# Kernel optimization log

Measured on AMD Instinct MI355X. Metric: run time of the kernel, lower is better.

The kernel has to match this reference:

```python
import jax, jax.numpy as jnp
import numpy as np

FEAT = 256
HID = 256
HEADS = 4
DH = HID // HEADS
SCALE = DH ** (-0.5)


def _linear(x, W, b):
    # torch nn.Linear convention: W is [out, in]
    return jnp.einsum('...i,oi->...o', x, W) + b


def _layernorm(x, gamma, beta, eps=1e-5):
    mu = jnp.mean(x, axis=-1, keepdims=True)
    var = jnp.mean(jnp.square(x - mu), axis=-1, keepdims=True)
    return (x - mu) * jax.lax.rsqrt(var + eps) * gamma + beta


def setup_inputs() -> dict:
    key = jax.random.key(0)
    ks = jax.random.split(key, 16)
    B, N = 4, 2048
    def w(k, shape, fan_in):
        return jax.random.uniform(k, shape, jnp.float32, -1.0, 1.0) / np.sqrt(fan_in)
    return {
        'x0': jax.random.normal(ks[0], (B, N, FEAT), jnp.float32),
        'x1': jax.random.normal(ks[1], (B, N, FEAT), jnp.float32),
        'Wqk': w(ks[2], (HID, FEAT), FEAT), 'bqk': w(ks[3], (HID,), FEAT),
        'Wv': w(ks[4], (HID, FEAT), FEAT), 'bv': w(ks[5], (HID,), FEAT),
        'Wp': w(ks[6], (HID, HID), HID), 'bp': w(ks[7], (HID,), HID),
        'W1': w(ks[8], (FEAT * 2, FEAT + HID), FEAT + HID), 'b1': w(ks[9], (FEAT * 2,), FEAT + HID),
        'gamma': jnp.ones((FEAT * 2,), jnp.float32), 'beta': jnp.zeros((FEAT * 2,), jnp.float32),
        'W2': w(ks[10], (FEAT, FEAT * 2), FEAT * 2), 'b2': w(ks[11], (FEAT,), FEAT * 2),
    }


def _forward(x0, x1, Wqk, bqk, Wv, bv, Wp, bp, W1, b1, gamma, beta, W2, b2):
    B, N0, _ = x0.shape
    N1 = x1.shape[1]

    def heads(t):  # [B, N, HID] -> [B, H, N, DH]
        return t.reshape(t.shape[0], t.shape[1], HEADS, DH).transpose(0, 2, 1, 3)

    qk0 = heads(_linear(x0, Wqk, bqk)) * (SCALE ** 0.5)
    qk1 = heads(_linear(x1, Wqk, bqk)) * (SCALE ** 0.5)
    v0 = heads(_linear(x0, Wv, bv))
    v1 = heads(_linear(x1, Wv, bv))

    sim = jnp.einsum('bhid,bhjd->bhij', qk0, qk1)  # [B,H,N0,N1]
    attn01 = jax.nn.softmax(sim, axis=-1)                      # rows over N1
    attn10 = jax.nn.softmax(sim.transpose(0, 1, 3, 2), axis=-1)  # [B,H,N1,N0], rows over N0

    m0 = jnp.einsum('bhij,bhjd->bhid', attn01, v1)  # [B,H,N0,DH]
    m1 = jnp.einsum('bhij,bhjd->bhid', attn10, v0)  # [B,H,N1,DH]

    def merge(t):  # [B,H,N,DH] -> [B,N,HID]
        return t.transpose(0, 2, 1, 3).reshape(t.shape[0], t.shape[2], HID)

    m0 = _linear(merge(m0), Wp, bp)
    m1 = _linear(merge(m1), Wp, bp)

    def mlp(x, m):
        h = _linear(jnp.concatenate([x, m], axis=-1), W1, b1)
        h = jax.nn.gelu(_layernorm(h, gamma, beta), approximate=False)
        return x + _linear(h, W2, b2)

    return mlp(x0, m0), mlp(x1, m1)


def reference(x0, x1, Wqk, bqk, Wv, bv, Wp, bp, W1, b1, gamma, beta, W2, b2):
    return _forward(x0, x1, Wqk, bqk, Wv, bv, Wp, bp, W1, b1, gamma, beta, W2, b2)
```

## Files before the change

### kernel.cpp

```cpp
#include <hip/hip_runtime.h>
#include <hip/hip_bf16.h>
#include <math.h>

typedef __hip_bfloat16 hbf;
typedef __attribute__((ext_vector_type(8))) short short8;
typedef __attribute__((ext_vector_type(4))) short short4v;
typedef __attribute__((ext_vector_type(4))) float f32x4;

#define ROWS 8192
#define SQSL 0.4246609001440095f
#define COFF 24.0f

__device__ __forceinline__ short f2b(float f) {
    union { hbf h; short s; } u; u.h = __float2bfloat16(f); return u.s;
}
__device__ __forceinline__ float b2f(short s) {
    union { unsigned u; float f; } x;
    x.u = ((unsigned)(unsigned short)s) << 16; return x.f;
}

__global__ __launch_bounds__(256)
void prep(const float* __restrict__ Wqk, const float* __restrict__ Wv,
          const float* __restrict__ Wp, const float* __restrict__ W1,
          const float* __restrict__ W2,
          const float* __restrict__ bp, const float* __restrict__ b1,
          short* __restrict__ wq, short* __restrict__ wv,
          short* __restrict__ w1c, short* __restrict__ w2,
          float* __restrict__ bc)
{
    const int bid = blockIdx.x, tid = threadIdx.x;
    if (bid < 512) {
        const float* src; short* dst; int base; float sc = 1.f;
        if (bid < 64)       { src = Wqk; dst = wq; base = bid;       sc = SQSL; }
        else if (bid < 128) { src = Wv;  dst = wv; base = bid - 64; }
        else if (bid < 384) {
            int i = (bid - 128) * 256 + tid;
            int n = i >> 7, c = (i & 127) * 4;
            if (c < 256) {
                float4 f = ((const float4*)W1)[i];
                short4v s;
                s[0] = f2b(f.x); s[1] = f2b(f.y); s[2] = f2b(f.z); s[3] = f2b(f.w);
                *(short4v*)(w1c + (size_t)n * 512 + c) = s;
            }
            return;
        }
        else                { src = W2;  dst = w2; base = bid - 384; }
        int i = base * 256 + tid;
        float4 f = ((const float4*)src)[i];
        short4v s;
        s[0] = f2b(f.x * sc); s[1] = f2b(f.y * sc);
        s[2] = f2b(f.z * sc); s[3] = f2b(f.w * sc);
        *(short4v*)(dst + (size_t)i * 4) = s;
    } else if (bid < 1024) {
        int n = bid - 512;
        const float* wrow = W1 + (size_t)n * 512 + 256;
        float acc = 0.f;
        for (int k = 0; k < 256; ++k)
            acc += wrow[k] * Wp[(size_t)k * 256 + tid];
        w1c[(size_t)n * 512 + 256 + tid] = f2b(acc);
    } else {
        int n = (bid - 1024) * 256 + tid;
        const float* wrow = W1 + (size_t)n * 512 + 256;
        float acc = b1[n];
        for (int k = 0; k < 256; ++k) acc += wrow[k] * bp[k];
        bc[n] = acc;
    }
}

__global__ __launch_bounds__(256)
void gemm_qkv(const float* __restrict__ x0, const float* __restrict__ x1,
              const short* __restrict__ Wa, const short* __restrict__ Wb,
              const float* __restrict__ bias0, const float* __restrict__ bias1,
              short* __restrict__ Cb, short* __restrict__ Cb2)
{
    const int col0 = blockIdx.x * 128;
    const int row0 = blockIdx.y * 64;
    const int tid = threadIdx.x;
    const int lane = tid & 63, wave = tid >> 6;
    const int ln = lane & 15, quad = lane >> 4;
    const int wm = wave & 1, wn = wave >> 1;

    __shared__ short As[64 * 40];
    __shared__ short Bs[128 * 40];

    const int ar = tid >> 2, ac = tid & 3;

    f32x4 acc[2][4];
    #pragma unroll
    for (int i = 0; i < 2; ++i)
        #pragma unroll
        for (int j = 0; j < 4; ++j) acc[i][j] = {0.f, 0.f, 0.f, 0.f};

    auto wptr = [&](int rr, int kk) -> const short* {
        int n = col0 + rr;
        if (col0 < 256) return Wa + (size_t)n * 256 + kk;
        return Wb + (size_t)(n - 256) * 256 + kk;
    };
    const float* xrow = (row0 + ar < ROWS)
        ? x0 + (size_t)(row0 + ar) * 256
        : x1 + (size_t)(row0 + ar - ROWS) * 256;

    float4 aF0 = ((const float4*)(xrow + ac * 8))[0];
    float4 aF1 = ((const float4*)(xrow + ac * 8))[1];
    short8 bR0 = *(const short8*)wptr(ar, ac * 8);
    short8 bR1 = *(const short8*)wptr(ar + 64, ac * 8);

    for (int k0 = 0; k0 < 256; k0 += 32) {
        {
            short8 s;
            s[0] = f2b(aF0.x); s[1] = f2b(aF0.y); s[2] = f2b(aF0.z); s[3] = f2b(aF0.w);
            s[4] = f2b(aF1.x); s[5] = f2b(aF1.y); s[6] = f2b(aF1.z); s[7] = f2b(aF1.w);
            *(short8*)&As[ar * 40 + ac * 8] = s;
        }
        *(short8*)&Bs[ar * 40 + ac * 8] = bR0;
        *(short8*)&Bs[(ar + 64) * 40 + ac * 8] = bR1;
        __syncthreads();

        if (k0 + 32 < 256) {
            aF0 = ((const float4*)(xrow + k0 + 32 + ac * 8))[0];
            aF1 = ((const float4*)(xrow + k0 + 32 + ac * 8))[1];
            bR0 = *(const short8*)wptr(ar, k0 + 32 + ac * 8);
            bR1 = *(const short8*)wptr(ar + 64, k0 + 32 + ac * 8);
        }

        short8 a[2], b[4];
        #pragma unroll
        for (int mi = 0; mi < 2; ++mi)
            a[mi] = *(const short8*)&As[(wm * 32 + mi * 16 + ln) * 40 + quad * 8];
        #pragma unroll
        for (int nj = 0; nj < 4; ++nj)
            b[nj] = *(const short8*)&Bs[(wn * 64 + nj * 16 + ln) * 40 + quad * 8];
        #pragma unroll
        for (int mi = 0; mi < 2; ++mi)
            #pragma unroll
            for (int nj = 0; nj < 4; ++nj)
                acc[mi][nj] = __builtin_amdgcn_mfma_f32_16x16x32_bf16(
                                  b[nj], a[mi], acc[mi][nj], 0, 0, 0);
        __syncthreads();
    }

    #pragma unroll
    for (int nj = 0; nj < 4; ++nj) {
        int wrel = wn * 64 + nj * 16 + quad * 4;
        int wcol = col0 + wrel;
        const float* bias = (wcol >= 256) ? bias1 : bias0;
        int boff = (wcol >= 256) ? (wcol - 256) : wcol;
        float4 bb = *(const float4*)(bias + boff);
        #pragma unroll
        for (int mi = 0; mi < 2; ++mi) {
            int tok = row0 + wm * 32 + mi * 16 + ln;
            f32x4 v = acc[mi][nj];
            short4v o;
            if (wcol < 256) {
                o[0] = f2b(fmaf(bb.x, SQSL, v[0])); o[1] = f2b(fmaf(bb.y, SQSL, v[1]));
                o[2] = f2b(fmaf(bb.z, SQSL, v[2])); o[3] = f2b(fmaf(bb.w, SQSL, v[3]));
                *(short4v*)(Cb + (size_t)tok * 256 + wcol) = o;
            } else {
                o[0] = f2b(v[0] + bb.x); o[1] = f2b(v[1] + bb.y);
                o[2] = f2b(v[2] + bb.z); o[3] = f2b(v[3] + bb.w);
                *(short4v*)(Cb2 + (size_t)tok * 256 + (wcol - 256)) = o;
            }
        }
    }
}

__global__ __launch_bounds__(256)
void vtrans(const short* __restrict__ vbuf, short* __restrict__ vtbuf)
{
    const int tt = blockIdx.x;
    const int gh = blockIdx.y;
    const int g = gh >> 2, h = gh & 3;
    const int tid = threadIdx.x;
    const int tok0 = g * 2048 + tt * 64;

    __shared__ short Ls[64 * 76];

    {
        int c4 = tid & 15, r0 = tid >> 4;
        #pragma unroll
        for (int gg = 0; gg < 4; ++gg) {
            int r = r0 + gg * 16;
            *(short4v*)&Ls[r * 76 + c4 * 4] =
                *(const short4v*)(vbuf + (size_t)(tok0 + r) * 256 + h * 64 + c4 * 4);
        }
    }
    __syncthreads();

    #pragma unroll
    for (int p = 0; p < 2; ++p) {
        int ch = tid + p * 256;
        int d = ch >> 3, cc = ch & 7;
        short8 s;
        #pragma unroll
        for (int j = 0; j < 8; ++j) s[j] = Ls[(cc * 8 + j) * 76 + d];
        *(short8*)(vtbuf + (size_t)((g * 4 + h) * 64 + d) * 2048 + tt * 64 + cc * 8) = s;
    }
}

__global__ __launch_bounds__(128, 2)
void attn8(const short* __restrict__ qkb, const short* __restrict__ vtbuf,
           short* __restrict__ pO0, short* __restrict__ pO1,
           float* __restrict__ l0, float* __restrict__ l1)
{
    const int qt   = blockIdx.x;
    const int b    = blockIdx.y >> 2, h = blockIdx.y & 3;
    const int dir  = blockIdx.z >> 1;
    const int half = blockIdx.z & 1;
    const int tid = threadIdx.x;
    const int lane = tid & 63, wave = tid >> 6;
    const int ln   = lane & 15, quad = lane >> 4;

    const int qbase = dir * ROWS + b * 2048;
    const int kbase = (1 - dir) * ROWS + b * 2048;
    const int vg    = ((1 - dir) * 4 + b) * 4 + h;
    const int jlo   = half * 1024, jhi = jlo + 1024;

    short* __restrict__ pO = half ? pO1 : pO0;
    float* __restrict__ lb = half ? l1  : l0;

    __shared__ short QP[128 * 72];
    __shared__ short KS[64 * 72];
    __shared__ short VT[64 * 72];

    const int c = tid & 7, r0 = tid >> 3;
    #pragma unroll
    for (int g = 0; g < 8; ++g) {
        int r = r0 + g * 16;
        *(short8*)&QP[r * 72 + c * 8] =
            *(const short8*)(qkb + (size_t)(qbase + qt * 128 + r) * 256 + h * 64 + c * 8);
    }
    #pragma unroll
    for (int g = 0; g < 4; ++g) {
        int r = r0 + g * 16;
        *(short8*)&KS[r * 72 + c * 8] =
            *(const short8*)(qkb + (size_t)(kbase + jlo + r) * 256 + h * 64 + c * 8);
        *(short8*)&VT[r * 72 + c * 8] =
            *(const short8*)(vtbuf + (size_t)(vg * 64 + r) * 2048 + jlo + c * 8);
    }
    __syncthreads();

    short8 qf[4][2];
    #pragma unroll
    for (int mi = 0; mi < 4; ++mi)
        #pragma unroll
        for (int ks = 0; ks < 2; ++ks)
            qf[mi][ks] = *(const short8*)&QP[(wave * 64 + mi * 16 + ln) * 72
                                             + ks * 32 + quad * 8];

    f32x4 Ot[4][4];
    #pragma unroll
    for (int mi = 0; mi < 4; ++mi)
        #pragma unroll
        for (int dt = 0; dt < 4; ++dt) Ot[mi][dt] = {0.f, 0.f, 0.f, 0.f};
    float lrun[4] = {0.f, 0.f, 0.f, 0.f};

    for (int j0 = jlo; j0 < jhi; j0 += 64) {
        short8 kreg[4], vreg[4];
        const bool more = (j0 + 64) < jhi;
        if (more) {
            #pragma unroll
            for (int g = 0; g < 4; ++g) {
                int r = r0 + g * 16;
                kreg[g] = *(const short8*)(qkb + (size_t)(kbase + j0 + 64 + r) * 256
                                           + h * 64 + c * 8);
                vreg[g] = *(const short8*)(vtbuf + (size_t)(vg * 64 + r) * 2048
                                           + j0 + 64 + c * 8);
            }
        }

        f32x4 St[4][4];
        #pragma unroll
        for (int t = 0; t < 4; ++t) {
            short8 k0 = *(const short8*)&KS[(t * 16 + ln) * 72 + quad * 8];
            short8 k1 = *(const short8*)&KS[(t * 16 + ln) * 72 + 32 + quad * 8];
            #pragma unroll
            for (int mi = 0; mi < 4; ++mi) {
                f32x4 z = {0.f, 0.f, 0.f, 0.f};
                z = __builtin_amdgcn_mfma_f32_16x16x32_bf16(k0, qf[mi][0], z, 0, 0, 0);
                St[mi][t] = __builtin_amdgcn_mfma_f32_16x16x32_bf16(k1, qf[mi][1], z, 0, 0, 0);
            }
        }

        float ss[4] = {0.f, 0.f, 0.f, 0.f};
        #pragma unroll
        for (int mi = 0; mi < 4; ++mi)
            #pragma unroll
            for (int t = 0; t < 4; ++t) {
                float p0 = __builtin_amdgcn_exp2f(St[mi][t][0] - COFF);
                float p1 = __builtin_amdgcn_exp2f(St[mi][t][1] - COFF);
                float p2 = __builtin_amdgcn_exp2f(St[mi][t][2] - COFF);
                float p3 = __builtin_amdgcn_exp2f(St[mi][t][3] - COFF);
                ss[mi] += (p0 + p1) + (p2 + p3);
                unsigned d0 = (__float_as_uint(p0) >> 16) |
                              (__float_as_uint(p1) & 0xffff0000u);
                unsigned d1 = (__float_as_uint(p2) >> 16) |
                              (__float_as_uint(p3) & 0xffff0000u);
                *(int2*)&QP[(wave * 64 + mi * 16 + ln) * 72 + t * 16 + quad * 4] =
                    make_int2((int)d0, (int)d1);
            }
        #pragma unroll
        for (int mi = 0; mi < 4; ++mi) {
            float t = ss[mi];
            t += __shfl_xor(t, 16);
            t += __shfl_xor(t, 32);
            lrun[mi] += t;
        }

        short8 pa[4][2];
        #pragma unroll
        for (int mi = 0; mi < 4; ++mi)
            #pragma unroll
            for (int ks = 0; ks < 2; ++ks)
                pa[mi][ks] = *(const short8*)&QP[(wave * 64 + mi * 16 + ln) * 72
                                                 + ks * 32 + quad * 8];
        #pragma unroll
        for (int dt = 0; dt < 4; ++dt) {
            short8 v0 = *(const short8*)&VT[(dt * 16 + ln) * 72 + quad * 8];
            short8 v1 = *(const short8*)&VT[(dt * 16 + ln) * 72 + 32 + quad * 8];
            #pragma unroll
            for (int mi = 0; mi < 4; ++mi) {
                Ot[mi][dt] = __builtin_amdgcn_mfma_f32_16x16x32_bf16(
                                 v0, pa[mi][0], Ot[mi][dt], 0, 0, 0);
                Ot[mi][dt] = __builtin_amdgcn_mfma_f32_16x16x32_bf16(
                                 v1, pa[mi][1], Ot[mi][dt], 0, 0, 0);
            }
        }
        __syncthreads();

        if (more) {
            #pragma unroll
            for (int g = 0; g < 4; ++g) {
                int r = r0 + g * 16;
                *(short8*)&KS[r * 72 + c * 8] = kreg[g];
                *(short8*)&VT[r * 72 + c * 8] = vreg[g];
            }
        }
        __syncthreads();
    }

    #pragma unroll
    for (int mi = 0; mi < 4; ++mi) {
        int tok = qbase + qt * 128 + wave * 64 + mi * 16 + ln;
        if (quad == 0) lb[tok] = lrun[mi];
        #pragma unroll
        for (int dt = 0; dt < 4; ++dt) {
            short4v o;
            #pragma unroll
            for (int r = 0; r < 4; ++r) o[r] = f2b(Ot[mi][dt][r]);
            *(short4v*)(pO + (size_t)tok * 256 + h * 64 + dt * 16 + quad * 4) = o;
        }
    }
}

__global__ __launch_bounds__(256)
void mlp_fused(const float* __restrict__ x0, const float* __restrict__ x1,
               const short* __restrict__ pO0, const short* __restrict__ pO1,
               const float* __restrict__ l0, const float* __restrict__ l1,
               const short* __restrict__ w1c, const short* __restrict__ w2,
               const float* __restrict__ bc, const float* __restrict__ gamma,
               const float* __restrict__ beta, const float* __restrict__ b2,
               float* __restrict__ out)
{
    const int tok0 = blockIdx.x * 32;
    const int tid = threadIdx.x;
    const int lane = tid & 63, wave = tid >> 6;
    const int ln = lane & 15, quad = lane >> 4;

    __shared__ short As[32 * 40];
    __shared__ short Bs[256 * 40];
    __shared__ short H [32 * 520];
    __shared__ float stats[4][2][32];

    f32x4 acc[2][8];
    #pragma unroll
    for (int i = 0; i < 2; ++i)
        #pragma unroll
        for (int j = 0; j < 8; ++j) acc[i][j] = {0.f, 0.f, 0.f, 0.f};

    const int br = tid >> 2, bcol = tid & 3;

    for (int k0 = 0; k0 < 512; k0 += 32) {
        #pragma unroll
        for (int p = 0; p < 2; ++p) {
            if (p == 0 && tid < 128) {
                int arow = tid >> 2, ac = tid & 3;
                int kk = k0 + ac * 8;
                int tok = tok0 + arow;
                short8 s;
                if (k0 < 256) {
                    const float* xr = (tok < ROWS ? x0 + (size_t)tok * 256
                                                  : x1 + (size_t)(tok - ROWS) * 256) + kk;
                    float4 f0 = ((const float4*)xr)[0];
                    float4 f1 = ((const float4*)xr)[1];
                    s[0] = f2b(f0.x); s[1] = f2b(f0.y); s[2] = f2b(f0.z); s[3] = f2b(f0.w);
                    s[4] = f2b(f1.x); s[5] = f2b(f1.y); s[6] = f2b(f1.z); s[7] = f2b(f1.w);
                } else {
                    short8 a = *(const short8*)(pO0 + (size_t)tok * 256 + (kk - 256));
                    short8 b = *(const short8*)(pO1 + (size_t)tok * 256 + (kk - 256));
                    float inv = __builtin_amdgcn_rcpf(l0[tok] + l1[tok]);
                    #pragma unroll
                    for (int j = 0; j < 8; ++j)
                        s[j] = f2b((b2f(a[j]) + b2f(b[j])) * inv);
                }
                *(short8*)&As[arow * 40 + ac * 8] = s;
            }
            #pragma unroll
            for (int q = 0; q < 4; ++q) {
                int r = br + q * 64;
                *(short8*)&Bs[r * 40 + bcol * 8] =
                    *(const short8*)(w1c + (size_t)(p * 256 + r) * 512 + k0 + bcol * 8);
            }
            __syncthreads();

            short8 a0 = *(const short8*)&As[ln * 40 + quad * 8];
            short8 a1 = *(const short8*)&As[(16 + ln) * 40 + quad * 8];
            #pragma unroll
            for (int nj = 0; nj < 4; ++nj) {
                short8 bf = *(const short8*)&Bs[(wave * 64 + nj * 16 + ln) * 40 + quad * 8];
                acc[0][p * 4 + nj] = __builtin_amdgcn_mfma_f32_16x16x32_bf16(
                                         bf, a0, acc[0][p * 4 + nj], 0, 0, 0);
                acc[1][p * 4 + nj] = __builtin_amdgcn_mfma_f32_16x16x32_bf16(
                                         bf, a1, acc[1][p * 4 + nj], 0, 0, 0);
            }
            __syncthreads();
        }
    }

    #pragma unroll
    for (int p = 0; p < 2; ++p)
        #pragma unroll
        for (int nj = 0; nj < 4; ++nj) {
            int hcol = p * 256 + wave * 64 + nj * 16 + quad * 4;
            float4 bb = *(const float4*)(bc + hcol);
            acc[0][p * 4 + nj][0] += bb.x; acc[1][p * 4 + nj][0] += bb.x;
            acc[0][p * 4 + nj][1] += bb.y; acc[1][p * 4 + nj][1] += bb.y;
            acc[0][p * 4 + nj][2] += bb.z; acc[1][p * 4 + nj][2] += bb.z;
            acc[0][p * 4 + nj][3] += bb.w; acc[1][p * 4 + nj][3] += bb.w;
        }

    #pragma unroll
    for (int mi = 0; mi < 2; ++mi) {
        float s1 = 0.f, s2 = 0.f;
        #pragma unroll
        for (int j = 0; j < 8; ++j)
            #pragma unroll
            for (int r = 0; r < 4; ++r) {
                float v = acc[mi][j][r];
                s1 += v; s2 += v * v;
            }
        s1 += __shfl_xor(s1, 16); s2 += __shfl_xor(s2, 16);
        s1 += __shfl_xor(s1, 32); s2 += __shfl_xor(s2, 32);
        if (quad == 0) {
            stats[wave][0][mi * 16 + ln] = s1;
            stats[wave][1][mi * 16 + ln] = s2;
        }
    }
    __syncthreads();

    float mean[2], rstd[2];
    #pragma unroll
    for (int mi = 0; mi < 2; ++mi) {
        int t = mi * 16 + ln;
        float s1 = stats[0][0][t] + stats[1][0][t] + stats[2][0][t] + stats[3][0][t];
        float s2 = stats[0][1][t] + stats[1][1][t] + stats[2][1][t] + stats[3][1][t];
        mean[mi] = s1 * (1.f / 512.f);
        float var = s2 * (1.f / 512.f) - mean[mi] * mean[mi];
        rstd[mi] = rsqrtf(var + 1e-5f);
    }

    #pragma unroll
    for (int p = 0; p < 2; ++p)
        #pragma unroll
        for (int nj = 0; nj < 4; ++nj) {
            int hcol = p * 256 + wave * 64 + nj * 16 + quad * 4;
            float4 gm = *(const float4*)(gamma + hcol);
            float4 bt = *(const float4*)(beta + hcol);
            #pragma unroll
            for (int mi = 0; mi < 2; ++mi) {
                short4v o;
                #pragma unroll
                for (int r = 0; r < 4; ++r) {
                    float g = (r == 0) ? gm.x : (r == 1) ? gm.y : (r == 2) ? gm.z : gm.w;
                    float bta = (r == 0) ? bt.x : (r == 1) ? bt.y : (r == 2) ? bt.z : bt.w;
                    float y = (acc[mi][p * 4 + nj][r] - mean[mi]) * rstd[mi] * g + bta;
                    float u = y * fmaf(y * y, 0.0356774081f, 0.7978845608f);
                    float e = __builtin_amdgcn_exp2f(u * -2.8853900818f);
                    o[r] = f2b(y * __builtin_amdgcn_rcpf(1.f + e));
                }
                *(short4v*)&H[(mi * 16 + ln) * 520 + hcol] = o;
            }
        }
    __syncthreads();

    f32x4 acc2[2][4];
    #pragma unroll
    for (int i = 0; i < 2; ++i)
        #pragma unroll
        for (int j = 0; j < 4; ++j) acc2[i][j] = {0.f, 0.f, 0.f, 0.f};

    for (int k0 = 0; k0 < 512; k0 += 32) {
        #pragma unroll
        for (int q = 0; q < 4; ++q) {
            int r = br + q * 64;
            *(short8*)&Bs[r * 40 + bcol * 8] =
                *(const short8*)(w2 + (size_t)r * 512 + k0 + bcol * 8);
        }
        __syncthreads();

        short8 h0 = *(const short8*)&H[ln * 520 + k0 + quad * 8];
        short8 h1 = *(const short8*)&H[(16 + ln) * 520 + k0 + quad * 8];
        #pragma unroll
        for (int nj = 0; nj < 4; ++nj) {
            short8 wf = *(const short8*)&Bs[(wave * 64 + nj * 16 + ln) * 40 + quad * 8];
            acc2[0][nj] = __builtin_amdgcn_mfma_f32_16x16x32_bf16(wf, h0, acc2[0][nj], 0, 0, 0);
            acc2[1][nj] = __builtin_amdgcn_mfma_f32_16x16x32_bf16(wf, h1, acc2[1][nj], 0, 0, 0);
        }
        __syncthreads();
    }

    #pragma unroll
    for (int nj = 0; nj < 4; ++nj) {
        int ocol = wave * 64 + nj * 16 + quad * 4;
        float4 bb = *(const float4*)(b2 + ocol);
        #pragma unroll
        for (int mi = 0; mi < 2; ++mi) {
            int tok = tok0 + mi * 16 + ln;
            const float* xr = (tok < ROWS ? x0 + (size_t)tok * 256
                                          : x1 + (size_t)(tok - ROWS) * 256);
            float4 rv = *(const float4*)(xr + ocol);
            float4 o;
            o.x = acc2[mi][nj][0] + bb.x + rv.x;
            o.y = acc2[mi][nj][1] + bb.y + rv.y;
            o.z = acc2[mi][nj][2] + bb.z + rv.z;
            o.w = acc2[mi][nj][3] + bb.w + rv.w;
            *(float4*)(out + (size_t)tok * 256 + ocol) = o;
        }
    }
}

extern "C" void kernel_launch(void* const* d_in, const int* in_sizes, int n_in,
                              void* d_out, int out_size, void* d_ws, size_t ws_size,
                              hipStream_t stream)
{
    const float* x0    = (const float*)d_in[0];
    const float* x1    = (const float*)d_in[1];
    const float* Wqk   = (const float*)d_in[2];
    const float* bqk   = (const float*)d_in[3];
    const float* Wv    = (const float*)d_in[4];
    const float* bv    = (const float*)d_in[5];
    const float* Wp    = (const float*)d_in[6];
    const float* bp    = (const float*)d_in[7];
    const float* W1    = (const float*)d_in[8];
    const float* b1    = (const float*)d_in[9];
    const float* gamma = (const float*)d_in[10];
    const float* beta  = (const float*)d_in[11];
    const float* W2    = (const float*)d_in[12];
    const float* b2    = (const float*)d_in[13];
    float* out = (float*)d_out;

    char* ws = (char*)d_ws;
    const size_t MB = 1024 * 1024;
    short* qkb  = (short*)ws;
    short* vtb  = (short*)(ws + 8  * MB);
    short* pO0  = (short*)(ws + 16 * MB);
    short* pO1  = (short*)(ws + 24 * MB);
    short* vbuf = pO1;
    float* l0   = (float*)(ws + 32 * MB);
    float* l1   = l0 + 16384;
    float* bc   = l1 + 16384;
    short* wq   = (short*)(bc + 512);
    short* wv   = wq + 65536;
    short* w1c  = wv + 65536;
    short* w2   = w1c + 262144;

    prep<<<1026, 256, 0, stream>>>(Wqk, Wv, Wp, W1, W2, bp, b1,
                                   wq, wv, w1c, w2, bc);
    gemm_qkv<<<dim3(4, 256), 256, 0, stream>>>(x0, x1, wq, wv, bqk, bv, qkb, vbuf);
    vtrans<<<dim3(32, 32), 256, 0, stream>>>(vbuf, vtb);
    attn8<<<dim3(16, 16, 4), 128, 0, stream>>>(qkb, vtb, pO0, pO1, l0, l1);
    mlp_fused<<<512, 256, 0, stream>>>(x0, x1, pO0, pO1, l0, l1, w1c, w2, bc,
                                       gamma, beta, b2, out);
}
```

Measured before the change: 221.2 us.

## Fuse V transpose into QKV GEMM, deepen K tiles, remap grids, prefetch MLP weights

Folds the V transpose into the QKV GEMM epilogue through shared memory, so the separate vtrans kernel and its global round trip are removed. Widens the K step from 32 to 64 in the QKV GEMM and both MLP GEMMs, and adds register prefetch of the next weight tile in the MLP. The MLP now stages the full concatenated input row into shared memory once instead of per K step. It also remaps block indices in gemm_qkv and attn8 for better locality and raises wave priority around the MFMA sections. In exchange it uses more shared memory and registers, which may lower occupancy.

Result: faster. 202.2 us (-8.6%).

```diff
diff --git a/kernel.cpp b/kernel.cpp
--- a/kernel.cpp
+++ b/kernel.cpp
@@ -71,17 +71,20 @@
 void gemm_qkv(const float* __restrict__ x0, const float* __restrict__ x1,
               const short* __restrict__ Wa, const short* __restrict__ Wb,
               const float* __restrict__ bias0, const float* __restrict__ bias1,
-              short* __restrict__ Cb, short* __restrict__ Cb2)
+              short* __restrict__ qkb, short* __restrict__ vtb)
 {
-    const int col0 = blockIdx.x * 128;
-    const int row0 = blockIdx.y * 64;
+    const int fid  = blockIdx.x + (blockIdx.y << 2);
+    const int col0 = (fid >> 8) * 128;
+    const int row0 = (fid & 255) * 64;
     const int tid = threadIdx.x;
     const int lane = tid & 63, wave = tid >> 6;
     const int ln = lane & 15, quad = lane >> 4;
     const int wm = wave & 1, wn = wave >> 1;
 
-    __shared__ short As[64 * 40];
-    __shared__ short Bs[128 * 40];
+    __shared__ short smem[64 * 72 + 128 * 72];
+    short* As = smem;
+    short* Bs = smem + 64 * 72;
+    short* Vt = smem;
 
     const int ar = tid >> 2, ac = tid & 3;
 
@@ -91,109 +94,113 @@
         #pragma unroll
         for (int j = 0; j < 4; ++j) acc[i][j] = {0.f, 0.f, 0.f, 0.f};
 
-    auto wptr = [&](int rr, int kk) -> const short* {
-        int n = col0 + rr;
-        if (col0 < 256) return Wa + (size_t)n * 256 + kk;
-        return Wb + (size_t)(n - 256) * 256 + kk;
-    };
+    const short* wbase = (col0 < 256) ? Wa + (size_t)col0 * 256
+                                      : Wb + (size_t)(col0 - 256) * 256;
     const float* xrow = (row0 + ar < ROWS)
         ? x0 + (size_t)(row0 + ar) * 256
         : x1 + (size_t)(row0 + ar - ROWS) * 256;
 
-    float4 aF0 = ((const float4*)(xrow + ac * 8))[0];
-    float4 aF1 = ((const float4*)(xrow + ac * 8))[1];
-    short8 bR0 = *(const short8*)wptr(ar, ac * 8);
-    short8 bR1 = *(const short8*)wptr(ar + 64, ac * 8);
-
-    for (int k0 = 0; k0 < 256; k0 += 32) {
+    float4 aF[4];
+    short8 bR[4];
+    #pragma unroll
+    for (int i = 0; i < 4; ++i) aF[i] = ((const float4*)(xrow + ac * 16))[i];
+    bR[0] = *(const short8*)(wbase + (size_t)ar * 256 + ac * 16);
+    bR[1] = *(const short8*)(wbase + (size_t)ar * 256 + ac * 16 + 8);
+    bR[2] = *(const short8*)(wbase + (size_t)(ar + 64) * 256 + ac * 16);
+    bR[3] = *(const short8*)(wbase + (size_t)(ar + 64) * 256 + ac * 16 + 8);
+
+    for (int k0 = 0; k0 < 256; k0 += 64) {
         {
-            short8 s;
-            s[0] = f2b(aF0.x); s[1] = f2b(aF0.y); s[2] = f2b(aF0.z); s[3] = f2b(aF0.w);
-            s[4] = f2b(aF1.x); s[5] = f2b(aF1.y); s[6] = f2b(aF1.z); s[7] = f2b(aF1.w);
-            *(short8*)&As[ar * 40 + ac * 8] = s;
-        }
-        *(short8*)&Bs[ar * 40 + ac * 8] = bR0;
-        *(short8*)&Bs[(ar + 64) * 40 + ac * 8] = bR1;
+            short8 s0, s1;
+            s0[0] = f2b(aF[0].x); s0[1] = f2b(aF[0].y); s0[2] = f2b(aF[0].z); s0[3] = f2b(aF[0].w);
+            s0[4] = f2b(aF[1].x); s0[5] = f2b(aF[1].y); s0[6] = f2b(aF[1].z); s0[7] = f2b(aF[1].w);
+            s1[0] = f2b(aF[2].x); s1[1] = f2b(aF[2].y); s1[2] = f2b(aF[2].z); s1[3] = f2b(aF[2].w);
+            s1[4] = f2b(aF[3].x); s1[5] = f2b(aF[3].y); s1[6] = f2b(aF[3].z); s1[7] = f2b(aF[3].w);
+            *(short8*)&As[ar * 72 + ac * 16]     = s0;
+            *(short8*)&As[ar * 72 + ac * 16 + 8] = s1;
+        }
+        *(short8*)&Bs[ar * 72 + ac * 16]            = bR[0];
+        *(short8*)&Bs[ar * 72 + ac * 16 + 8]        = bR[1];
+        *(short8*)&Bs[(ar + 64) * 72 + ac * 16]     = bR[2];
+        *(short8*)&Bs[(ar + 64) * 72 + ac * 16 + 8] = bR[3];
         __syncthreads();
 
-        if (k0 + 32 < 256) {
-            aF0 = ((const float4*)(xrow + k0 + 32 + ac * 8))[0];
-            aF1 = ((const float4*)(xrow + k0 + 32 + ac * 8))[1];
-            bR0 = *(const short8*)wptr(ar, k0 + 32 + ac * 8);
-            bR1 = *(const short8*)wptr(ar + 64, k0 + 32 + ac * 8);
-        }
-
-        short8 a[2], b[4];
+        if (k0 + 64 < 256) {
+            const int kk = k0 + 64 + ac * 16;
+            #pragma unroll
+            for (int i = 0; i < 4; ++i) aF[i] = ((const float4*)(xrow + kk))[i];
+            bR[0] = *(const short8*)(wbase + (size_t)ar * 256 + kk);
+            bR[1] = *(const short8*)(wbase + (size_t)ar * 256 + kk + 8);
+            bR[2] = *(const short8*)(wbase + (size_t)(ar + 64) * 256 + kk);
+            bR[3] = *(const short8*)(wbase + (size_t)(ar + 64) * 256 + kk + 8);
+        }
+
+        short8 a[2][2], b[4][2];
         #pragma unroll
         for (int mi = 0; mi < 2; ++mi)
-            a[mi] = *(const short8*)&As[(wm * 32 + mi * 16 + ln) * 40 + quad * 8];
+            #pragma unroll
+            for (int ks = 0; ks < 2; ++ks)
+                a[mi][ks] = *(const short8*)&As[(wm * 32 + mi * 16 + ln) * 72 + ks * 32 + quad * 8];
         #pragma unroll
         for (int nj = 0; nj < 4; ++nj)
-            b[nj] = *(const short8*)&Bs[(wn * 64 + nj * 16 + ln) * 40 + quad * 8];
+            #pragma unroll
+            for (int ks = 0; ks < 2; ++ks)
+                b[nj][ks] = *(const short8*)&Bs[(wn * 64 + nj * 16 + ln) * 72 + ks * 32 + quad * 8];
         #pragma unroll
         for (int mi = 0; mi < 2; ++mi)
             #pragma unroll
-            for (int nj = 0; nj < 4; ++nj)
+            for (int nj = 0; nj < 4; ++nj) {
                 acc[mi][nj] = __builtin_amdgcn_mfma_f32_16x16x32_bf16(
-                                  b[nj], a[mi], acc[mi][nj], 0, 0, 0);
+                                  b[nj][0], a[mi][0], acc[mi][nj], 0, 0, 0);
+                acc[mi][nj] = __builtin_amdgcn_mfma_f32_16x16x32_bf16(
+                                  b[nj][1], a[mi][1], acc[mi][nj], 0, 0, 0);
+            }
         __syncthreads();
     }
 
-    #pragma unroll
-    for (int nj = 0; nj < 4; ++nj) {
-        int wrel = wn * 64 + nj * 16 + quad * 4;
-        int wcol = col0 + wrel;
-        const float* bias = (wcol >= 256) ? bias1 : bias0;
-        int boff = (wcol >= 256) ? (wcol - 256) : wcol;
-        float4 bb = *(const float4*)(bias + boff);
-        #pragma unroll
-        for (int mi = 0; mi < 2; ++mi) {
-            int tok = row0 + wm * 32 + mi * 16 + ln;
-            f32x4 v = acc[mi][nj];
-            short4v o;
-            if (wcol < 256) {
-                o[0] = f2b(fmaf(bb.x, SQSL, v[0])); o[1] = f2b(fmaf(bb.y, SQSL, v[1]));
-                o[2] = f2b(fmaf(bb.z, SQSL, v[2])); o[3] = f2b(fmaf(bb.w, SQSL, v[3]));
-                *(short4v*)(Cb + (size_t)tok * 256 + wcol) = o;
-            } else {
-                o[0] = f2b(v[0] + bb.x); o[1] = f2b(v[1] + bb.y);
-                o[2] = f2b(v[2] + bb.z); o[3] = f2b(v[3] + bb.w);
-                *(short4v*)(Cb2 + (size_t)tok * 256 + (wcol - 256)) = o;
-            }
-        }
-    }
-}
-
-__global__ __launch_bounds__(256)
-void vtrans(const short* __restrict__ vbuf, short* __restrict__ vtbuf)
-{
-    const int tt = blockIdx.x;
-    const int gh = blockIdx.y;
-    const int g = gh >> 2, h = gh & 3;
-    const int tid = threadIdx.x;
-    const int tok0 = g * 2048 + tt * 64;
-
-    __shared__ short Ls[64 * 76];
-
-    {
-        int c4 = tid & 15, r0 = tid >> 4;
-        #pragma unroll
-        for (int gg = 0; gg < 4; ++gg) {
-            int r = r0 + gg * 16;
-            *(short4v*)&Ls[r * 76 + c4 * 4] =
-                *(const short4v*)(vbuf + (size_t)(tok0 + r) * 256 + h * 64 + c4 * 4);
-        }
-    }
-    __syncthreads();
-
-    #pragma unroll
-    for (int p = 0; p < 2; ++p) {
-        int ch = tid + p * 256;
-        int d = ch >> 3, cc = ch & 7;
-        short8 s;
-        #pragma unroll
-        for (int j = 0; j < 8; ++j) s[j] = Ls[(cc * 8 + j) * 76 + d];
-        *(short8*)(vtbuf + (size_t)((g * 4 + h) * 64 + d) * 2048 + tt * 64 + cc * 8) = s;
+    if (col0 < 256) {
+        #pragma unroll
+        for (int nj = 0; nj < 4; ++nj) {
+            const int wcol = col0 + wn * 64 + nj * 16 + quad * 4;
+            float4 bb = *(const float4*)(bias0 + wcol);
+            #pragma unroll
+            for (int mi = 0; mi < 2; ++mi) {
+                const int tok = row0 + wm * 32 + mi * 16 + ln;
+                f32x4 v = acc[mi][nj];
+                short4v o;
+                o[0] = f2b(fmaf(bb.x, SQSL, v[0]));
+                o[1] = f2b(fmaf(bb.y, SQSL, v[1]));
+                o[2] = f2b(fmaf(bb.z, SQSL, v[2]));
+                o[3] = f2b(fmaf(bb.w, SQSL, v[3]));
+                *(short4v*)(qkb + (size_t)tok * 256 + wcol) = o;
+            }
+        }
+    } else {
+        #pragma unroll
+        for (int nj = 0; nj < 4; ++nj) {
+            const int wrel = wn * 64 + nj * 16 + quad * 4;
+            float4 bb = *(const float4*)(bias1 + (col0 - 256) + wrel);
+            #pragma unroll
+            for (int mi = 0; mi < 2; ++mi) {
+                const int tl = wm * 32 + mi * 16 + ln;
+                f32x4 v = acc[mi][nj];
+                Vt[(wrel + 0) * 72 + tl] = f2b(v[0] + bb.x);
+                Vt[(wrel + 1) * 72 + tl] = f2b(v[1] + bb.y);
+                Vt[(wrel + 2) * 72 + tl] = f2b(v[2] + bb.z);
+                Vt[(wrel + 3) * 72 + tl] = f2b(v[3] + bb.w);
+            }
+        }
+        __syncthreads();
+        {
+            const int g4 = (row0 >> 11) * 4, tc0 = row0 & 2047;
+            const int r = tid >> 1, hf = tid & 1;
+            const int vcol = (col0 - 256) + r;
+            const int hh = vcol >> 6, d = vcol & 63;
+            short* dst = vtb + (size_t)((g4 + hh) * 64 + d) * 2048 + tc0 + hf * 32;
+            #pragma unroll
+            for (int cc = 0; cc < 4; ++cc)
+                *(short8*)(dst + cc * 8) = *(const short8*)&Vt[r * 72 + hf * 32 + cc * 8];
+        }
     }
 }
 
@@ -202,10 +209,12 @@
            short* __restrict__ pO0, short* __restrict__ pO1,
            float* __restrict__ l0, float* __restrict__ l1)
 {
-    const int qt   = blockIdx.x;
-    const int b    = blockIdx.y >> 2, h = blockIdx.y & 3;
-    const int dir  = blockIdx.z >> 1;
-    const int half = blockIdx.z & 1;
+    const int nfl = blockIdx.x + (blockIdx.y << 4) + (blockIdx.z << 8);
+    const int qt  = nfl >> 6;
+    const int gg  = nfl & 63;
+    const int b    = (gg >> 2) & 3, h = gg & 3;
+    const int dir  = gg >> 5;
+    const int half = (gg >> 4) & 1;
     const int tid = threadIdx.x;
     const int lane = tid & 63, wave = tid >> 6;
     const int ln   = lane & 15, quad = lane >> 4;
@@ -269,6 +278,7 @@
         }
 
         f32x4 St[4][4];
+        __builtin_amdgcn_s_setprio(1);
         #pragma unroll
         for (int t = 0; t < 4; ++t) {
             short8 k0 = *(const short8*)&KS[(t * 16 + ln) * 72 + quad * 8];
@@ -280,6 +290,7 @@
                 St[mi][t] = __builtin_amdgcn_mfma_f32_16x16x32_bf16(k1, qf[mi][1], z, 0, 0, 0);
             }
         }
+        __builtin_amdgcn_s_setprio(0);
 
         float ss[4] = {0.f, 0.f, 0.f, 0.f};
         #pragma unroll
@@ -313,6 +324,7 @@
             for (int ks = 0; ks < 2; ++ks)
                 pa[mi][ks] = *(const short8*)&QP[(wave * 64 + mi * 16 + ln) * 72
                                                  + ks * 32 + quad * 8];
+        __builtin_amdgcn_s_setprio(1);
         #pragma unroll
         for (int dt = 0; dt < 4; ++dt) {
             short8 v0 = *(const short8*)&VT[(dt * 16 + ln) * 72 + quad * 8];
@@ -325,6 +337,7 @@
                                  v1, pa[mi][1], Ot[mi][dt], 0, 0, 0);
             }
         }
+        __builtin_amdgcn_s_setprio(0);
         __syncthreads();
 
         if (more) {
@@ -366,65 +379,96 @@
     const int lane = tid & 63, wave = tid >> 6;
     const int ln = lane & 15, quad = lane >> 4;
 
-    __shared__ short As[32 * 40];
-    __shared__ short Bs[256 * 40];
     __shared__ short H [32 * 520];
+    __shared__ short Bs[256 * 72];
     __shared__ float stats[4][2][32];
 
+    const int br = tid >> 2, bq = tid & 3;
+    short8 bp[8];
+    auto loadB = [&](const short* W, int rw, int k0) {
+        const short* src = W + (size_t)(rw + br) * 512 + k0 + bq * 16;
+        #pragma unroll
+        for (int q = 0; q < 4; ++q) {
+            bp[2 * q]     = *(const short8*)(src + (size_t)q * 64 * 512);
+            bp[2 * q + 1] = *(const short8*)(src + (size_t)q * 64 * 512 + 8);
+        }
+    };
+    loadB(w1c, 0, 0);
+
+    {
+        const int arow = tid >> 3, ac = tid & 7;
+        const int tok = tok0 + arow;
+        if (ac < 4) {
+            const float* xr = (tok < ROWS ? x0 + (size_t)tok * 256
+                                          : x1 + (size_t)(tok - ROWS) * 256) + ac * 64;
+            #pragma unroll
+            for (int cc = 0; cc < 8; ++cc) {
+                float4 f0 = ((const float4*)(xr + cc * 8))[0];
+                float4 f1 = ((const float4*)(xr + cc * 8))[1];
+                short8 s;
+                s[0] = f2b(f0.x); s[1] = f2b(f0.y); s[2] = f2b(f0.z); s[3] = f2b(f0.w);
+                s[4] = f2b(f1.x); s[5] = f2b(f1.y); s[6] = f2b(f1.z); s[7] = f2b(f1.w);
+                *(short8*)&H[arow * 520 + ac * 64 + cc * 8] = s;
+            }
+        } else {
+            const int vc = (ac - 4) * 64;
+            const float inv = __builtin_amdgcn_rcpf(l0[tok] + l1[tok]);
+            #pragma unroll
+            for (int cc = 0; cc < 8; ++cc) {
+                short8 a = *(const short8*)(pO0 + (size_t)tok * 256 + vc + cc * 8);
+                short8 b = *(const short8*)(pO1 + (size_t)tok * 256 + vc + cc * 8);
+                short8 s;
+                #pragma unroll
+                for (int j = 0; j < 8; ++j)
+                    s[j] = f2b((b2f(a[j]) + b2f(b[j])) * inv);
+                *(short8*)&H[arow * 520 + 256 + vc + cc * 8] = s;
+            }
+        }
+    }
+
     f32x4 acc[2][8];
     #pragma unroll
     for (int i = 0; i < 2; ++i)
         #pragma unroll
         for (int j = 0; j < 8; ++j) acc[i][j] = {0.f, 0.f, 0.f, 0.f};
 
-    const int br = tid >> 2, bcol = tid & 3;
-
-    for (int k0 = 0; k0 < 512; k0 += 32) {
+    __syncthreads();
+
+    for (int k2 = 0; k2 < 8; ++k2) {
+        const int k0 = k2 * 64;
+        short8 a0[2], a1[2];
+        #pragma unroll
+        for (int ks = 0; ks < 2; ++ks) {
+            a0[ks] = *(const short8*)&H[ln * 520 + k0 + ks * 32 + quad * 8];
+            a1[ks] = *(const short8*)&H[(16 + ln) * 520 + k0 + ks * 32 + quad * 8];
+        }
         #pragma unroll
         for (int p = 0; p < 2; ++p) {
-            if (p == 0 && tid < 128) {
-                int arow = tid >> 2, ac = tid & 3;
-                int kk = k0 + ac * 8;
-                int tok = tok0 + arow;
-                short8 s;
-                if (k0 < 256) {
-                    const float* xr = (tok < ROWS ? x0 + (size_t)tok * 256
-                                                  : x1 + (size_t)(tok - ROWS) * 256) + kk;
-                    float4 f0 = ((const float4*)xr)[0];
-                    float4 f1 = ((const float4*)xr)[1];
-                    s[0] = f2b(f0.x); s[1] = f2b(f0.y); s[2] = f2b(f0.z); s[3] = f2b(f0.w);
-                    s[4] = f2b(f1.x); s[5] = f2b(f1.y); s[6] = f2b(f1.z); s[7] = f2b(f1.w);
-                } else {
-                    short8 a = *(const short8*)(pO0 + (size_t)tok * 256 + (kk - 256));
-                    short8 b = *(const short8*)(pO1 + (size_t)tok * 256 + (kk - 256));
-                    float inv = __builtin_amdgcn_rcpf(l0[tok] + l1[tok]);
-                    #pragma unroll
-                    for (int j = 0; j < 8; ++j)
-                        s[j] = f2b((b2f(a[j]) + b2f(b[j])) * inv);
+            #pragma unroll
+            for (int q = 0; q < 4; ++q) {
+                *(short8*)&Bs[(br + q * 64) * 72 + bq * 16]     = bp[2 * q];
+                *(short8*)&Bs[(br + q * 64) * 72 + bq * 16 + 8] = bp[2 * q + 1];
+            }
+            __syncthreads();
+            if (p == 0)          loadB(w1c, 256, k0);
+            else if (k2 < 7)     loadB(w1c, 0, k0 + 64);
+            #pragma unroll
+            for (int nj = 0; nj < 4; ++nj) {
+                #pragma unroll
+                for (int ks = 0; ks < 2; ++ks) {
+                    short8 bf = *(const short8*)&Bs[(wave * 64 + nj * 16 + ln) * 72
+                                                    + ks * 32 + quad * 8];
+                    acc[0][p * 4 + nj] = __builtin_amdgcn_mfma_f32_16x16x32_bf16(
+                                             bf, a0[ks], acc[0][p * 4 + nj], 0, 0, 0);
+                    acc[1][p * 4 + nj] = __builtin_amdgcn_mfma_f32_16x16x32_bf16(
+                                             bf, a1[ks], acc[1][p * 4 + nj], 0, 0, 0);
                 }
-                *(short8*)&As[arow * 40 + ac * 8] = s;
-            }
-            #pragma unroll
-            for (int q = 0; q < 4; ++q) {
-                int r = br + q * 64;
-                *(short8*)&Bs[r * 40 + bcol * 8] =
-                    *(const short8*)(w1c + (size_t)(p * 256 + r) * 512 + k0 + bcol * 8);
             }
             __syncthreads();
-
-            short8 a0 = *(const short8*)&As[ln * 40 + quad * 8];
-            short8 a1 = *(const short8*)&As[(16 + ln) * 40 + quad * 8];
-            #pragma unroll
-            for (int nj = 0; nj < 4; ++nj) {
-                short8 bf = *(const short8*)&Bs[(wave * 64 + nj * 16 + ln) * 40 + quad * 8];
-                acc[0][p * 4 + nj] = __builtin_amdgcn_mfma_f32_16x16x32_bf16(
-                                         bf, a0, acc[0][p * 4 + nj], 0, 0, 0);
-                acc[1][p * 4 + nj] = __builtin_amdgcn_mfma_f32_16x16x32_bf16(
-                                         bf, a1, acc[1][p * 4 + nj], 0, 0, 0);
-            }
-            __syncthreads();
-        }
-    }
+        }
+    }
+
+    loadB(w2, 0, 0);
 
     #pragma unroll
     for (int p = 0; p < 2; ++p)
@@ -490,7 +534,6 @@
                 *(short4v*)&H[(mi * 16 + ln) * 520 + hcol] = o;
             }
         }
-    __syncthreads();
 
     f32x4 acc2[2][4];
     #pragma unroll
@@ -498,22 +541,32 @@
         #pragma unroll
         for (int j = 0; j < 4; ++j) acc2[i][j] = {0.f, 0.f, 0.f, 0.f};
 
-    for (int k0 = 0; k0 < 512; k0 += 32) {
+    for (int s = 0; s < 8; ++s) {
+        const int k0 = s * 64;
         #pragma unroll
         for (int q = 0; q < 4; ++q) {
-            int r = br + q * 64;
-            *(short8*)&Bs[r * 40 + bcol * 8] =
-                *(const short8*)(w2 + (size_t)r * 512 + k0 + bcol * 8);
+            *(short8*)&Bs[(br + q * 64) * 72 + bq * 16]     = bp[2 * q];
+            *(short8*)&Bs[(br + q * 64) * 72 + bq * 16 + 8] = bp[2 * q + 1];
         }
         __syncthreads();
-
-        short8 h0 = *(const short8*)&H[ln * 520 + k0 + quad * 8];
-        short8 h1 = *(const short8*)&H[(16 + ln) * 520 + k0 + quad * 8];
+        if (s < 7) loadB(w2, 0, k0 + 64);
+        short8 h0[2], h1[2];
+        #pragma unroll
+        for (int ks = 0; ks < 2; ++ks) {
+            h0[ks] = *(const short8*)&H[ln * 520 + k0 + ks * 32 + quad * 8];
+            h1[ks] = *(const short8*)&H[(16 + ln) * 520 + k0 + ks * 32 + quad * 8];
+        }
         #pragma unroll
         for (int nj = 0; nj < 4; ++nj) {
-            short8 wf = *(const short8*)&Bs[(wave * 64 + nj * 16 + ln) * 40 + quad * 8];
-            acc2[0][nj] = __builtin_amdgcn_mfma_f32_16x16x32_bf16(wf, h0, acc2[0][nj], 0, 0, 0);
-            acc2[1][nj] = __builtin_amdgcn_mfma_f32_16x16x32_bf16(wf, h1, acc2[1][nj], 0, 0, 0);
+            #pragma unroll
+            for (int ks = 0; ks < 2; ++ks) {
+                short8 wf = *(const short8*)&Bs[(wave * 64 + nj * 16 + ln) * 72
+                                                + ks * 32 + quad * 8];
+                acc2[0][nj] = __builtin_amdgcn_mfma_f32_16x16x32_bf16(
+                                  wf, h0[ks], acc2[0][nj], 0, 0, 0);
+                acc2[1][nj] = __builtin_amdgcn_mfma_f32_16x16x32_bf16(
+                                  wf, h1[ks], acc2[1][nj], 0, 0, 0);
+            }
         }
         __syncthreads();
     }
@@ -564,7 +617,6 @@
     short* vtb  = (short*)(ws + 8  * MB);
     short* pO0  = (short*)(ws + 16 * MB);
     short* pO1  = (short*)(ws + 24 * MB);
-    short* vbuf = pO1;
     float* l0   = (float*)(ws + 32 * MB);
     float* l1   = l0 + 16384;
     float* bc   = l1 + 16384;
@@ -575,8 +627,7 @@
 
     prep<<<1026, 256, 0, stream>>>(Wqk, Wv, Wp, W1, W2, bp, b1,
                                    wq, wv, w1c, w2, bc);
-    gemm_qkv<<<dim3(4, 256), 256, 0, stream>>>(x0, x1, wq, wv, bqk, bv, qkb, vbuf);
-    vtrans<<<dim3(32, 32), 256, 0, stream>>>(vbuf, vtb);
+    gemm_qkv<<<dim3(4, 256), 256, 0, stream>>>(x0, x1, wq, wv, bqk, bv, qkb, vtb);
     attn8<<<dim3(16, 16, 4), 128, 0, stream>>>(qkb, vtb, pO0, pO1, l0, l1);
     mlp_fused<<<512, 256, 0, stream>>>(x0, x1, pO0, pO1, l0, l1, w1c, w2, bc,
                                        gamma, beta, b2, out);
```
